# Optimization experiments

Hardware: AMD Instinct MI355X
Metric: run time of the kernel (lower is better)

## Reference

```python
import jax, jax.numpy as jnp
import numpy as np

B, S, D = 2, 1024, 768
H, DH = 12, 64
M = 64            # performer random features
DFF = 4 * D
EPS_LN = 1e-5
EPS_PHI = 1e-6


def setup_inputs() -> dict:
    key = jax.random.key(0)
    ks = jax.random.split(key, 12)
    std = 0.02
    return {
        "x": jax.random.normal(ks[0], (B, S, D), jnp.float32),
        "ln1_g": jnp.ones((D,), jnp.float32),
        "ln1_b": jnp.zeros((D,), jnp.float32),
        "w_attn": jax.random.normal(ks[1], (D, 3 * D), jnp.float32) * std,
        "b_attn": jnp.zeros((3 * D,), jnp.float32),
        "w_feat": jax.random.normal(ks[2], (M, DH), jnp.float32),  # FAVOR+ projection
        "w_proj": jax.random.normal(ks[3], (D, D), jnp.float32) * std,
        "b_proj": jnp.zeros((D,), jnp.float32),
        "ln2_g": jnp.ones((D,), jnp.float32),
        "ln2_b": jnp.zeros((D,), jnp.float32),
        "w_fc": jax.random.normal(ks[4], (D, DFF), jnp.float32) * std,
        "b_fc": jnp.zeros((DFF,), jnp.float32),
        "w_out": jax.random.normal(ks[5], (DFF, D), jnp.float32) * std,
        "b_out": jnp.zeros((D,), jnp.float32),
    }


def _layernorm(x, g, b):
    mu = jnp.mean(x, axis=-1, keepdims=True)
    var = jnp.mean(jnp.square(x - mu), axis=-1, keepdims=True)
    return (x - mu) * jax.lax.rsqrt(var + EPS_LN) * g + b


def _phi(x, w_feat):
    # FAVOR+ positive softmax-kernel features. x: [B,H,S,DH] (already scaled by dh^-1/4)
    proj = jnp.einsum('bhsd,md->bhsm', x, w_feat)
    sq = 0.5 * jnp.sum(jnp.square(x), axis=-1, keepdims=True)
    return jnp.exp(proj - sq) / np.sqrt(M) + EPS_PHI


def _performer_attn(q, k, v, w_feat, w_proj, b_proj):
    # split heads: [B,S,D] -> [B,H,S,DH]
    def heads(t):
        return t.reshape(B, S, H, DH).transpose(0, 2, 1, 3)
    q, k, v = heads(q), heads(k), heads(v)
    scale = DH ** -0.25
    phi_q = _phi(q * scale, w_feat)  # [B,H,S,M]
    phi_k = _phi(k * scale, w_feat)
    # causal linear attention via prefix sums
    kv = jnp.cumsum(phi_k[..., :, None] * v[..., None, :], axis=2)  # [B,H,S,M,DH]
    num = jnp.einsum('bhsm,bhsmd->bhsd', phi_q, kv)
    den = jnp.einsum('bhsm,bhsm->bhs', phi_q, jnp.cumsum(phi_k, axis=2))
    out = num / den[..., None]
    out = out.transpose(0, 2, 1, 3).reshape(B, S, D)
    return out @ w_proj + b_proj


def reference(x, ln1_g, ln1_b, w_attn, b_attn, w_feat, w_proj, b_proj,
              ln2_g, ln2_b, w_fc, b_fc, w_out, b_out):
    a = _layernorm(x, ln1_g, ln1_b)
    qkv = a @ w_attn + b_attn                      # TFConv1D
    q, k, v = jnp.split(qkv, 3, axis=2)
    x = x + _performer_attn(q, k, v, w_feat, w_proj, b_proj)
    m = _layernorm(x, ln2_g, ln2_b)
    m = jax.nn.gelu(m @ w_fc + b_fc, approximate=True) @ w_out + b_out
    return x + m
```

## Files before the change

kernel.cpp:

```cpp
#include <hip/hip_runtime.h>
#include <hip/hip_bf16.h>
#include <math.h>

#define BB 2
#define SS 1024
#define DD 768
#define HH 12
#define DHH 64
#define MM 64
#define DFF 3072
#define BS (BB*SS)
#define EPS_LN 1e-5f
#define EPS_PHI 1e-6f
#define CC 64
#define NC (SS/CC)
#define NQ 3840
#define PQOFF 2304
#define PKOFF 3072
#define VOFF  1536

typedef __hip_bfloat16 bf16;
using v8s = __attribute__((ext_vector_type(8))) short;
using v4f = __attribute__((ext_vector_type(4))) float;
struct b4 { bf16 v[4]; };

typedef const __attribute__((address_space(1))) void ga_void;
typedef __attribute__((address_space(3))) void ls_void;
__device__ __forceinline__ void gload16(const void* g, void* l) {
    __builtin_amdgcn_global_load_lds((ga_void*)g, (ls_void*)l, 16, 0, 0);
}

__global__ __launch_bounds__(256) void prep_kernel(const float* __restrict__ w_attn,
                                                   const float* __restrict__ w_proj,
                                                   const float* __restrict__ w_fc,
                                                   const float* __restrict__ w_out,
                                                   const float* __restrict__ b_attn,
                                                   const float* __restrict__ wfeat,
                                                   bf16* __restrict__ wext_t,
                                                   bf16* __restrict__ wproj_t,
                                                   bf16* __restrict__ wfc_t,
                                                   bf16* __restrict__ wout_t,
                                                   float* __restrict__ bias_ext) {
    __shared__ float smem[2 * 64 * 65];
    int bid = blockIdx.x;
    int t = threadIdx.x;
    if (bid < 1728) {
        const float* in; bf16* outp; int K, N, xt, yt;
        if (bid < 432)       { in = w_attn; outp = wext_t;  K = 768;  N = 2304; xt = bid % 36; yt = bid / 36; }
        else if (bid < 576)  { int b = bid - 432;  in = w_proj; outp = wproj_t; K = 768;  N = 768;  xt = b % 12; yt = b / 12; }
        else if (bid < 1152) { int b = bid - 576;  in = w_fc;   outp = wfc_t;   K = 768;  N = 3072; xt = b % 48; yt = b / 48; }
        else                 { int b = bid - 1152; in = w_out;  outp = wout_t;  K = 3072; N = 768;  xt = b % 12; yt = b / 12; }
        float (*sm)[65] = (float(*)[65])smem;
        int n0 = xt * 64, k0 = yt * 64;
        int rr = t >> 4, cc = (t & 15) * 4;
        #pragma unroll
        for (int it = 0; it < 4; it++) {
            int kr = it * 16 + rr;
            float4 v = *(const float4*)&in[(size_t)(k0 + kr) * N + n0 + cc];
            sm[kr][cc + 0] = v.x; sm[kr][cc + 1] = v.y;
            sm[kr][cc + 2] = v.z; sm[kr][cc + 3] = v.w;
        }
        __syncthreads();
        #pragma unroll
        for (int it = 0; it < 4; it++) {
            int nr = it * 16 + rr;
            b4 o;
            #pragma unroll
            for (int j = 0; j < 4; j++) o.v[j] = __float2bfloat16(sm[cc + j][nr]);
            *(b4*)&outp[(size_t)(n0 + nr) * K + k0 + cc] = o;
        }
    } else if (bid < 2016) {
        int b2 = bid - 1728;
        int jb = b2 % 12, h = (b2 / 12) % 12, isK = b2 / 144;
        float (*wfT)[65] = (float(*)[65])smem;
        float (*Wt)[65]  = (float(*)[65])(smem + 64 * 65);
        int j0 = jb * 64;
        int base = isK * DD + h * DHH;
        const float scale = 0.35355339059327373f;
        #pragma unroll
        for (int it = 0; it < 16; it++) {
            int idx = it * 256 + t;
            int m = idx >> 6, d = idx & 63;
            wfT[d][m] = scale * wfeat[m * DHH + d];
            Wt[idx >> 6][idx & 63] = w_attn[(size_t)(j0 + (idx >> 6)) * (3 * DD) + base + (idx & 63)];
        }
        __syncthreads();
        int jl = t & 63, mg = (t >> 6) * 16;
        for (int m = mg; m < mg + 16; m++) {
            float acc = 0.f;
            #pragma unroll 8
            for (int d = 0; d < 64; d++) acc += wfT[d][m] * Wt[jl][d];
            wext_t[(size_t)(PQOFF + isK * DD + h * DHH + m) * DD + j0 + jl] = __float2bfloat16(acc);
        }
        if (jb == 0 && t < 64) {
            float accb = 0.f;
            #pragma unroll 8
            for (int d = 0; d < 64; d++) accb += wfT[d][t] * b_attn[base + d];
            bias_ext[PQOFF + isK * DD + h * DHH + t] = accb;
        }
    } else {
        for (int i = t; i < 3 * DD; i += 256) bias_ext[i] = b_attn[i];
    }
}

__global__ __launch_bounds__(256) void ln_kernel(const float* __restrict__ x,
                                                 const float* __restrict__ g,
                                                 const float* __restrict__ bta,
                                                 bf16* __restrict__ out) {
    int row = blockIdx.x;
    int t = threadIdx.x;
    const float* xr = x + (size_t)row * DD;
    float v0 = xr[t], v1 = xr[t + 256], v2 = xr[t + 512];
    float s = v0 + v1 + v2;
    float s2 = v0 * v0 + v1 * v1 + v2 * v2;
    #pragma unroll
    for (int off = 32; off > 0; off >>= 1) {
        s  += __shfl_xor(s,  off, 64);
        s2 += __shfl_xor(s2, off, 64);
    }
    __shared__ float ls[4], ls2[4];
    if ((t & 63) == 0) { ls[t >> 6] = s; ls2[t >> 6] = s2; }
    __syncthreads();
    s  = ls[0] + ls[1] + ls[2] + ls[3];
    s2 = ls2[0] + ls2[1] + ls2[2] + ls2[3];
    float mu  = s * (1.0f / DD);
    float var = s2 * (1.0f / DD) - mu * mu;
    float r = rsqrtf(var + EPS_LN);
    bf16* orow = out + (size_t)row * DD;
    orow[t]       = __float2bfloat16((v0 - mu) * r * g[t]       + bta[t]);
    orow[t + 256] = __float2bfloat16((v1 - mu) * r * g[t + 256] + bta[t + 256]);
    orow[t + 512] = __float2bfloat16((v2 - mu) * r * g[t + 512] + bta[t + 512]);
}

__device__ inline void swizzle44(int bid, int nx4, int& bx, int& by) {
    int g = bid >> 4, r = bid & 15;
    bx = (g % nx4) * 4 + (r & 3);
    by = (g / nx4) * 4 + (r >> 2);
}

__device__ inline float gelu_tanh(float x) {
    float x3 = x * x * x;
    float u = 0.7978845608028654f * (x + 0.044715f * x3);
    return 0.5f * x * (1.0f + tanhf(u));
}

template <int ACT, int HAS_RES, int OUT_BF16>
__global__ __launch_bounds__(256) void gemm_k128(const bf16* __restrict__ A,
                                                 const bf16* __restrict__ BT,
                                                 const float* __restrict__ bias,
                                                 const float* __restrict__ res,
                                                 void* __restrict__ Cout,
                                                 int N, int K, int nx4) {
    __shared__ bf16 Asl[64][128];
    __shared__ bf16 Bsl[64][128];
    int bx, by;
    swizzle44(blockIdx.x, nx4, bx, by);
    int tid = threadIdx.x;
    int m0 = by * 64, n0 = bx * 64;
    int wave = tid >> 6, lane = tid & 63;
    int qm = lane & 15, quad = lane >> 4;
    int srow = lane >> 4;
    int chnk = lane & 15;
    int sce = (chnk ^ srow) * 8;
    int sco = (chnk ^ (srow + 4)) * 8;
    const bf16* ag = A  + (size_t)(m0 + wave * 16 + srow) * K;
    const bf16* bg = BT + (size_t)(n0 + wave * 16 + srow) * K;
    int xr = (qm & 7) << 3;

    v4f acc[4] = {{0.f,0.f,0.f,0.f},{0.f,0.f,0.f,0.f},{0.f,0.f,0.f,0.f},{0.f,0.f,0.f,0.f}};

    for (int k0 = 0; k0 < K; k0 += 128) {
        __syncthreads();
        #pragma unroll
        for (int i = 0; i < 4; i++) {
            int sc = (i & 1) ? sco : sce;
            gload16(ag + (size_t)(4 * i) * K + k0 + sc, &Asl[wave * 16 + 4 * i][0]);
            gload16(bg + (size_t)(4 * i) * K + k0 + sc, &Bsl[wave * 16 + 4 * i][0]);
        }
        __syncthreads();
        #pragma unroll
        for (int kc = 0; kc < 4; kc++) {
            v8s a = *(const v8s*)&Asl[wave * 16 + qm][(kc * 32 + quad * 8) ^ xr];
            #pragma unroll
            for (int n = 0; n < 4; n++) {
                v8s b = *(const v8s*)&Bsl[n * 16 + qm][(kc * 32 + quad * 8) ^ xr];
                acc[n] = __builtin_amdgcn_mfma_f32_16x16x32_bf16(a, b, acc[n], 0, 0, 0);
            }
        }
    }

    int col_l = lane & 15;
    #pragma unroll
    for (int t = 0; t < 4; t++) {
        int col = n0 + t * 16 + col_l;
        float bcol = bias[col];
        #pragma unroll
        for (int r = 0; r < 4; r++) {
            int row = m0 + wave * 16 + quad * 4 + r;
            float v = acc[t][r] + bcol;
            if (ACT == 1) v = gelu_tanh(v);
            if (HAS_RES) v += res[(size_t)row * N + col];
            if (OUT_BF16) ((bf16*)Cout)[(size_t)row * N + col] = __float2bfloat16(v);
            else          ((float*)Cout)[(size_t)row * N + col] = v;
        }
    }
}

template <int ACT, int HAS_RES, int OUT_BF16>
__global__ __launch_bounds__(256) void gemm_m32_k128(const bf16* __restrict__ A,
                                                     const bf16* __restrict__ BT,
                                                     const float* __restrict__ bias,
                                                     const float* __restrict__ res,
                                                     void* __restrict__ Cout,
                                                     int N, int K, int nx4) {
    __shared__ bf16 Asl[32][128];
    __shared__ bf16 Bsl[64][128];
    int bx, by;
    swizzle44(blockIdx.x, nx4, bx, by);
    int tid = threadIdx.x;
    int m0 = by * 32, n0 = bx * 64;
    int wave = tid >> 6, lane = tid & 63;
    int qm = lane & 15, quad = lane >> 4;
    int rowh = (wave & 1) * 16;
    int colh = (wave >> 1) * 32;
    int srow = lane >> 4;
    int chnk = lane & 15;
    int sce = (chnk ^ srow) * 8;
    int sco = (chnk ^ (srow + 4)) * 8;
    const bf16* ag = A  + (size_t)(m0 + wave * 8  + srow) * K;
    const bf16* bg = BT + (size_t)(n0 + wave * 16 + srow) * K;
    int xr = (qm & 7) << 3;

    v4f acc[2] = {{0.f,0.f,0.f,0.f},{0.f,0.f,0.f,0.f}};

    for (int k0 = 0; k0 < K; k0 += 128) {
        __syncthreads();
        #pragma unroll
        for (int i = 0; i < 2; i++) {
            int sc = (i & 1) ? sco : sce;
            gload16(ag + (size_t)(4 * i) * K + k0 + sc, &Asl[wave * 8 + 4 * i][0]);
        }
        #pragma unroll
        for (int i = 0; i < 4; i++) {
            int sc = (i & 1) ? sco : sce;
            gload16(bg + (size_t)(4 * i) * K + k0 + sc, &Bsl[wave * 16 + 4 * i][0]);
        }
        __syncthreads();
        #pragma unroll
        for (int kc = 0; kc < 4; kc++) {
            v8s a  = *(const v8s*)&Asl[rowh + qm][(kc * 32 + quad * 8) ^ xr];
            v8s b0 = *(const v8s*)&Bsl[colh + qm][(kc * 32 + quad * 8) ^ xr];
            v8s b1 = *(const v8s*)&Bsl[colh + 16 + qm][(kc * 32 + quad * 8) ^ xr];
            acc[0] = __builtin_amdgcn_mfma_f32_16x16x32_bf16(a, b0, acc[0], 0, 0, 0);
            acc[1] = __builtin_amdgcn_mfma_f32_16x16x32_bf16(a, b1, acc[1], 0, 0, 0);
        }
    }

    #pragma unroll
    for (int ct = 0; ct < 2; ct++) {
        int col = n0 + colh + ct * 16 + qm;
        float bcol = bias[col];
        #pragma unroll
        for (int r = 0; r < 4; r++) {
            int row = m0 + rowh + quad * 4 + r;
            float v = acc[ct][r] + bcol;
            if (ACT == 1) v = gelu_tanh(v);
            if (HAS_RES) v += res[(size_t)row * N + col];
            if (OUT_BF16) ((bf16*)Cout)[(size_t)row * N + col] = __float2bfloat16(v);
            else          ((float*)Cout)[(size_t)row * N + col] = v;
        }
    }
}

__device__ __forceinline__ float rowsq16(b4 raw) {
    float sq = 0.f;
    #pragma unroll
    for (int j = 0; j < 4; j++) { float f = __bfloat162float(raw.v[j]); sq += f * f; }
    sq += __shfl_xor(sq, 1, 64); sq += __shfl_xor(sq, 2, 64);
    sq += __shfl_xor(sq, 4, 64); sq += __shfl_xor(sq, 8, 64);
    return sq * (1.0f / 16.0f);
}

__global__ __launch_bounds__(256) void scan_sums_mfma(const bf16* __restrict__ qkvp,
                                                      float* __restrict__ StateT,
                                                      float* __restrict__ Sk) {
    int c = blockIdx.x, h = blockIdx.y, b = blockIdx.z;
    int bh = b * HH + h;
    int t = threadIdx.x;
    __shared__ bf16 vt[64][72];
    __shared__ bf16 kt[64][72];
    int sr = t >> 4, cq = (t & 15) * 4;
    #pragma unroll
    for (int i = 0; i < 4; i++) {
        int s = sr + 16 * i;
        size_t rowg = ((size_t)b * SS + c * CC + s) * NQ + h * DHH;
        b4 vv = *(const b4*)&qkvp[rowg + VOFF  + cq];
        b4 kr = *(const b4*)&qkvp[rowg + DD    + cq];
        b4 kp = *(const b4*)&qkvp[rowg + PKOFF + cq];
        float sq = rowsq16(kr);
        #pragma unroll
        for (int j = 0; j < 4; j++) {
            vt[cq + j][s] = vv.v[j];
            kt[cq + j][s] = __float2bfloat16(
                __expf(__bfloat162float(kp.v[j]) - sq) * 0.125f + EPS_PHI);
        }
    }
    __syncthreads();
    int wave = t >> 6, lane = t & 63, qm = lane & 15, quad = lane >> 4;
    v4f acc[4] = {{0.f,0.f,0.f,0.f},{0.f,0.f,0.f,0.f},{0.f,0.f,0.f,0.f},{0.f,0.f,0.f,0.f}};
    #pragma unroll
    for (int k0 = 0; k0 < 64; k0 += 32) {
        v8s a = *(const v8s*)&vt[wave * 16 + qm][k0 + quad * 8];
        #pragma unroll
        for (int n = 0; n < 4; n++) {
            v8s bb = *(const v8s*)&kt[n * 16 + qm][k0 + quad * 8];
            acc[n] = __builtin_amdgcn_mfma_f32_16x16x32_bf16(a, bb, acc[n], 0, 0, 0);
        }
    }
    float* dst = StateT + ((size_t)bh * NC + c) * 4096;
    int col_l = lane & 15;
    #pragma unroll
    for (int n = 0; n < 4; n++)
        #pragma unroll
        for (int r = 0; r < 4; r++) {
            int d = wave * 16 + quad * 4 + r;
            dst[d * 64 + n * 16 + col_l] = acc[n][r];
        }
    if (t < 64) {
        float sum = 0.f;
        #pragma unroll 8
        for (int i = 0; i < 64; i++) sum += __bfloat162float(kt[t][i]);
        Sk[((size_t)bh * NC + c) * 64 + t] = sum;
    }
}

__global__ __launch_bounds__(256) void scan_prefix_kernel(float* __restrict__ Skv,
                                                          float* __restrict__ Sk) {
    int bh = blockIdx.y;
    int t = blockIdx.x * 256 + threadIdx.x;
    size_t base = (size_t)bh * NC * 4096 + t;
    float acc = 0.f;
    for (int c = 0; c < NC; c++) {
        float v = Skv[base + (size_t)c * 4096];
        Skv[base + (size_t)c * 4096] = acc;
        acc += v;
    }
    if (blockIdx.x == 0 && threadIdx.x < 64) {
        size_t b2 = (size_t)bh * NC * 64 + threadIdx.x;
        float a2 = 0.f;
        for (int c = 0; c < NC; c++) {
            float v = Sk[b2 + (size_t)c * 64];
            Sk[b2 + (size_t)c * 64] = a2;
            a2 += v;
        }
    }
}

__global__ __launch_bounds__(256) void scan_chunk_mfma(const bf16* __restrict__ qkvp,
                                                       const float* __restrict__ StateT,
                                                       const float* __restrict__ SkPre,
                                                       bf16* __restrict__ attn) {
    int c = blockIdx.x, h = blockIdx.y, b = blockIdx.z;
    int bh = b * HH + h;
    int t = threadIdx.x;
    __shared__ bf16 qs[64][72];
    __shared__ bf16 ks[64][72];
    __shared__ bf16 vt[80][72];
    __shared__ bf16 stl[80][72];
    __shared__ bf16 P[64][72];
    int sr = t >> 4, cq = (t & 15) * 4;
    const float* stg = StateT + ((size_t)bh * NC + c) * 4096;
    #pragma unroll
    for (int i = 0; i < 4; i++) {
        int s = sr + 16 * i;
        size_t rowg = ((size_t)b * SS + c * CC + s) * NQ + h * DHH;
        b4 qr = *(const b4*)&qkvp[rowg + 0     + cq];
        b4 qp = *(const b4*)&qkvp[rowg + PQOFF + cq];
        b4 kr = *(const b4*)&qkvp[rowg + DD    + cq];
        b4 kp = *(const b4*)&qkvp[rowg + PKOFF + cq];
        b4 vv = *(const b4*)&qkvp[rowg + VOFF  + cq];
        float4 sv = *(const float4*)&stg[s * 64 + cq];
        float sqq = rowsq16(qr);
        float sqk = rowsq16(kr);
        #pragma unroll
        for (int j = 0; j < 4; j++) {
            qs[s][cq + j] = __float2bfloat16(
                __expf(__bfloat162float(qp.v[j]) - sqq) * 0.125f + EPS_PHI);
            ks[s][cq + j] = __float2bfloat16(
                __expf(__bfloat162float(kp.v[j]) - sqk) * 0.125f + EPS_PHI);
            vt[cq + j][s] = vv.v[j];
        }
        stl[s][cq + 0] = __float2bfloat16(sv.x);
        stl[s][cq + 1] = __float2bfloat16(sv.y);
        stl[s][cq + 2] = __float2bfloat16(sv.z);
        stl[s][cq + 3] = __float2bfloat16(sv.w);
    }
    {
        int rr = 64 + (t >> 4);
        bf16 one = __float2bfloat16(rr == 64 ? 1.f : 0.f);
        vt[rr][cq + 0] = one; vt[rr][cq + 1] = one;
        vt[rr][cq + 2] = one; vt[rr][cq + 3] = one;
        if (rr == 64) {
            const float* skp = SkPre + ((size_t)bh * NC + c) * 64;
            float4 s4 = *(const float4*)&skp[cq];
            stl[64][cq + 0] = __float2bfloat16(s4.x);
            stl[64][cq + 1] = __float2bfloat16(s4.y);
            stl[64][cq + 2] = __float2bfloat16(s4.z);
            stl[64][cq + 3] = __float2bfloat16(s4.w);
        } else {
            bf16 z = __float2bfloat16(0.f);
            stl[rr][cq + 0] = z; stl[rr][cq + 1] = z;
            stl[rr][cq + 2] = z; stl[rr][cq + 3] = z;
        }
    }
    __syncthreads();
    int wave = t >> 6, lane = t & 63, qm = lane & 15, quad = lane >> 4;
    int col_l = lane & 15;
    int row0 = wave * 16;

    v4f a1[4] = {{0.f,0.f,0.f,0.f},{0.f,0.f,0.f,0.f},{0.f,0.f,0.f,0.f},{0.f,0.f,0.f,0.f}};
    #pragma unroll
    for (int k0 = 0; k0 < 64; k0 += 32) {
        v8s a = *(const v8s*)&qs[row0 + qm][k0 + quad * 8];
        #pragma unroll
        for (int n = 0; n < 4; n++) {
            v8s bb = *(const v8s*)&ks[n * 16 + qm][k0 + quad * 8];
            a1[n] = __builtin_amdgcn_mfma_f32_16x16x32_bf16(a, bb, a1[n], 0, 0, 0);
        }
    }
    #pragma unroll
    for (int n = 0; n < 4; n++)
        #pragma unroll
        for (int r = 0; r < 4; r++) {
            int row = row0 + quad * 4 + r;
            int col = n * 16 + col_l;
            float v = (col <= row) ? a1[n][r] : 0.f;
            P[row][col] = __float2bfloat16(v);
        }
    v4f acc[5] = {{0.f,0.f,0.f,0.f},{0.f,0.f,0.f,0.f},{0.f,0.f,0.f,0.f},
                  {0.f,0.f,0.f,0.f},{0.f,0.f,0.f,0.f}};
    #pragma unroll
    for (int k0 = 0; k0 < 64; k0 += 32) {
        v8s aq = *(const v8s*)&qs[row0 + qm][k0 + quad * 8];
        v8s ap = *(const v8s*)&P [row0 + qm][k0 + quad * 8];
        #pragma unroll
        for (int n = 0; n < 5; n++) {
            v8s b1 = *(const v8s*)&stl[n * 16 + qm][k0 + quad * 8];
            v8s b2 = *(const v8s*)&vt [n * 16 + qm][k0 + quad * 8];
            acc[n] = __builtin_amdgcn_mfma_f32_16x16x32_bf16(aq, b1, acc[n], 0, 0, 0);
            acc[n] = __builtin_amdgcn_mfma_f32_16x16x32_bf16(ap, b2, acc[n], 0, 0, 0);
        }
    }
    float den[4];
    #pragma unroll
    for (int r = 0; r < 4; r++)
        den[r] = __shfl(acc[4][r], (lane >> 4) << 4, 64);
    #pragma unroll
    for (int n = 0; n < 4; n++)
        #pragma unroll
        for (int r = 0; r < 4; r++) {
            int srow = row0 + quad * 4 + r;
            int d = n * 16 + col_l;
            attn[((size_t)b * SS + c * CC + srow) * DD + h * DHH + d] =
                __float2bfloat16(acc[n][r] / den[r]);
        }
}

extern "C" void kernel_launch(void* const* d_in, const int* in_sizes, int n_in,
                              void* d_out, int out_size, void* d_ws, size_t ws_size,
                              hipStream_t stream) {
    const float* x      = (const float*)d_in[0];
    const float* ln1_g  = (const float*)d_in[1];
    const float* ln1_b  = (const float*)d_in[2];
    const float* w_attn = (const float*)d_in[3];
    const float* b_attn = (const float*)d_in[4];
    const float* w_feat = (const float*)d_in[5];
    const float* w_proj = (const float*)d_in[6];
    const float* b_proj = (const float*)d_in[7];
    const float* ln2_g  = (const float*)d_in[8];
    const float* ln2_b  = (const float*)d_in[9];
    const float* w_fc   = (const float*)d_in[10];
    const float* b_fc   = (const float*)d_in[11];
    const float* w_out  = (const float*)d_in[12];
    const float* b_out  = (const float*)d_in[13];
    float* out = (float*)d_out;

    float* ws = (float*)d_ws;
    size_t off = 0;
    float* buf_x1   = ws + off; off += (size_t)BS * DD;
    float* buf_sk   = ws + off; off += (size_t)BB * HH * NC * MM;
    float* bias_ext = ws + off; off += NQ;
    bf16* wb = (bf16*)(ws + off);
    size_t boff = 0;
    bf16* buf_qkvp    = wb + boff; boff += (size_t)BS * NQ;
    bf16* buf_a_bf    = wb + boff; boff += (size_t)BS * DD;
    bf16* buf_attn_bf = wb + boff; boff += (size_t)BS * DD;
    bf16* wext_t      = wb + boff; boff += (size_t)NQ * DD;
    bf16* wproj_t     = wb + boff; boff += (size_t)DD * DD;
    bf16* wfc_t       = wb + boff; boff += (size_t)DFF * DD;
    bf16* wout_t      = wb + boff; boff += (size_t)DD * DFF;
    float* buf_skv   = buf_x1;
    bf16*  buf_fc_bf = buf_qkvp;

    prep_kernel<<<2017, 256, 0, stream>>>(w_attn, w_proj, w_fc, w_out, b_attn, w_feat,
                                          wext_t, wproj_t, wfc_t, wout_t, bias_ext);
    ln_kernel<<<BS, 256, 0, stream>>>(x, ln1_g, ln1_b, buf_a_bf);
    gemm_k128<0, 0, 1><<<1920, 256, 0, stream>>>(
        buf_a_bf, wext_t, bias_ext, nullptr, buf_qkvp, NQ, DD, 15);
    scan_sums_mfma<<<dim3(NC, HH, BB), 256, 0, stream>>>(buf_qkvp, buf_skv, buf_sk);
    scan_prefix_kernel<<<dim3(4096 / 256, BB * HH), 256, 0, stream>>>(buf_skv, buf_sk);
    scan_chunk_mfma<<<dim3(NC, HH, BB), 256, 0, stream>>>(
        buf_qkvp, buf_skv, buf_sk, buf_attn_bf);
    gemm_m32_k128<0, 1, 0><<<768, 256, 0, stream>>>(
        buf_attn_bf, wproj_t, b_proj, x, buf_x1, DD, DD, 3);
    ln_kernel<<<BS, 256, 0, stream>>>(buf_x1, ln2_g, ln2_b, buf_a_bf);
    gemm_k128<1, 0, 1><<<1536, 256, 0, stream>>>(
        buf_a_bf, wfc_t, b_fc, nullptr, buf_fc_bf, DFF, DD, 12);
    gemm_m32_k128<0, 1, 0><<<768, 256, 0, stream>>>(
        buf_fc_bf, wout_t, b_out, buf_x1, out, DD, DFF, 3);
}
```

Measured before the change: 227.9 us.

## Fuse LN1 into prep, emit q/k squared norms from QKV GEMM epilogue

New measurement: 227.9 us. No clear change (-0.0%).

```diff
diff --git a/kernel.cpp b/kernel.cpp
--- a/kernel.cpp
+++ b/kernel.cpp
@@ -30,12 +30,16 @@
     __builtin_amdgcn_global_load_lds((ga_void*)g, (ls_void*)l, 16, 0, 0);
 }
 
-__global__ __launch_bounds__(256) void prep_kernel(const float* __restrict__ w_attn,
+__global__ __launch_bounds__(256) void prep_kernel(const float* __restrict__ x,
+                                                   const float* __restrict__ ln1_g,
+                                                   const float* __restrict__ ln1_b,
+                                                   const float* __restrict__ w_attn,
                                                    const float* __restrict__ w_proj,
                                                    const float* __restrict__ w_fc,
                                                    const float* __restrict__ w_out,
                                                    const float* __restrict__ b_attn,
                                                    const float* __restrict__ wfeat,
+                                                   bf16* __restrict__ a_bf,
                                                    bf16* __restrict__ wext_t,
                                                    bf16* __restrict__ wproj_t,
                                                    bf16* __restrict__ wfc_t,
@@ -44,12 +48,36 @@
     __shared__ float smem[2 * 64 * 65];
     int bid = blockIdx.x;
     int t = threadIdx.x;
-    if (bid < 1728) {
+    if (bid < 2048) {
+        int row = bid;
+        const float* xr = x + (size_t)row * DD;
+        float v0 = xr[t], v1 = xr[t + 256], v2 = xr[t + 512];
+        float s = v0 + v1 + v2;
+        float s2 = v0 * v0 + v1 * v1 + v2 * v2;
+        #pragma unroll
+        for (int off = 32; off > 0; off >>= 1) {
+            s  += __shfl_xor(s,  off, 64);
+            s2 += __shfl_xor(s2, off, 64);
+        }
+        float* ls = smem; float* ls2 = smem + 4;
+        if ((t & 63) == 0) { ls[t >> 6] = s; ls2[t >> 6] = s2; }
+        __syncthreads();
+        s  = ls[0] + ls[1] + ls[2] + ls[3];
+        s2 = ls2[0] + ls2[1] + ls2[2] + ls2[3];
+        float mu  = s * (1.0f / DD);
+        float var = s2 * (1.0f / DD) - mu * mu;
+        float r = rsqrtf(var + EPS_LN);
+        bf16* orow = a_bf + (size_t)row * DD;
+        orow[t]       = __float2bfloat16((v0 - mu) * r * ln1_g[t]       + ln1_b[t]);
+        orow[t + 256] = __float2bfloat16((v1 - mu) * r * ln1_g[t + 256] + ln1_b[t + 256]);
+        orow[t + 512] = __float2bfloat16((v2 - mu) * r * ln1_g[t + 512] + ln1_b[t + 512]);
+    } else if (bid < 3776) {
+        int b = bid - 2048;
         const float* in; bf16* outp; int K, N, xt, yt;
-        if (bid < 432)       { in = w_attn; outp = wext_t;  K = 768;  N = 2304; xt = bid % 36; yt = bid / 36; }
-        else if (bid < 576)  { int b = bid - 432;  in = w_proj; outp = wproj_t; K = 768;  N = 768;  xt = b % 12; yt = b / 12; }
-        else if (bid < 1152) { int b = bid - 576;  in = w_fc;   outp = wfc_t;   K = 768;  N = 3072; xt = b % 48; yt = b / 48; }
-        else                 { int b = bid - 1152; in = w_out;  outp = wout_t;  K = 3072; N = 768;  xt = b % 12; yt = b / 12; }
+        if (b < 432)       { in = w_attn; outp = wext_t;  K = 768;  N = 2304; xt = b % 36; yt = b / 36; }
+        else if (b < 576)  { int b1 = b - 432;  in = w_proj; outp = wproj_t; K = 768;  N = 768;  xt = b1 % 12; yt = b1 / 12; }
+        else if (b < 1152) { int b1 = b - 576;  in = w_fc;   outp = wfc_t;   K = 768;  N = 3072; xt = b1 % 48; yt = b1 / 48; }
+        else               { int b1 = b - 1152; in = w_out;  outp = wout_t;  K = 3072; N = 768;  xt = b1 % 12; yt = b1 / 12; }
         float (*sm)[65] = (float(*)[65])smem;
         int n0 = xt * 64, k0 = yt * 64;
         int rr = t >> 4, cc = (t & 15) * 4;
@@ -69,8 +97,8 @@
             for (int j = 0; j < 4; j++) o.v[j] = __float2bfloat16(sm[cc + j][nr]);
             *(b4*)&outp[(size_t)(n0 + nr) * K + k0 + cc] = o;
         }
-    } else if (bid < 2016) {
-        int b2 = bid - 1728;
+    } else if (bid < 4064) {
+        int b2 = bid - 3776;
         int jb = b2 % 12, h = (b2 / 12) % 12, isK = b2 / 144;
         float (*wfT)[65] = (float(*)[65])smem;
         float (*Wt)[65]  = (float(*)[65])(smem + 64 * 65);
@@ -144,13 +172,14 @@
     return 0.5f * x * (1.0f + tanhf(u));
 }
 
-template <int ACT, int HAS_RES, int OUT_BF16>
+template <int ACT, int HAS_RES, int OUT_BF16, int SQMODE>
 __global__ __launch_bounds__(256) void gemm_k128(const bf16* __restrict__ A,
                                                  const bf16* __restrict__ BT,
                                                  const float* __restrict__ bias,
                                                  const float* __restrict__ res,
                                                  void* __restrict__ Cout,
-                                                 int N, int K, int nx4) {
+                                                 int N, int K, int nx4,
+                                                 float* __restrict__ sqbuf) {
     __shared__ bf16 Asl[64][128];
     __shared__ bf16 Bsl[64][128];
     int bx, by;
@@ -190,14 +219,33 @@
     }
 
     int col_l = lane & 15;
-    #pragma unroll
-    for (int t = 0; t < 4; t++) {
-        int col = n0 + t * 16 + col_l;
+    if (SQMODE && n0 < 1536) {
+        int hidx = n0 >> 6;
+        #pragma unroll
+        for (int r = 0; r < 4; r++) {
+            float hsq = 0.f;
+            #pragma unroll
+            for (int t2 = 0; t2 < 4; t2++) {
+                float v = acc[t2][r] + bias[n0 + t2 * 16 + col_l];
+                hsq += v * v;
+            }
+            hsq += __shfl_xor(hsq, 1, 64); hsq += __shfl_xor(hsq, 2, 64);
+            hsq += __shfl_xor(hsq, 4, 64); hsq += __shfl_xor(hsq, 8, 64);
+            if (col_l == 0) {
+                int row = m0 + wave * 16 + quad * 4 + r;
+                sqbuf[row * 24 + hidx] = hsq * (1.0f / 16.0f);
+            }
+        }
+        return;
+    }
+    #pragma unroll
+    for (int t2 = 0; t2 < 4; t2++) {
+        int col = n0 + t2 * 16 + col_l;
         float bcol = bias[col];
         #pragma unroll
         for (int r = 0; r < 4; r++) {
             int row = m0 + wave * 16 + quad * 4 + r;
-            float v = acc[t][r] + bcol;
+            float v = acc[t2][r] + bcol;
             if (ACT == 1) v = gelu_tanh(v);
             if (HAS_RES) v += res[(size_t)row * N + col];
             if (OUT_BF16) ((bf16*)Cout)[(size_t)row * N + col] = __float2bfloat16(v);
@@ -272,16 +320,8 @@
     }
 }
 
-__device__ __forceinline__ float rowsq16(b4 raw) {
-    float sq = 0.f;
-    #pragma unroll
-    for (int j = 0; j < 4; j++) { float f = __bfloat162float(raw.v[j]); sq += f * f; }
-    sq += __shfl_xor(sq, 1, 64); sq += __shfl_xor(sq, 2, 64);
-    sq += __shfl_xor(sq, 4, 64); sq += __shfl_xor(sq, 8, 64);
-    return sq * (1.0f / 16.0f);
-}
-
 __global__ __launch_bounds__(256) void scan_sums_mfma(const bf16* __restrict__ qkvp,
+                                                      const float* __restrict__ sqbuf,
                                                       float* __restrict__ StateT,
                                                       float* __restrict__ Sk) {
     int c = blockIdx.x, h = blockIdx.y, b = blockIdx.z;
@@ -293,11 +333,11 @@
     #pragma unroll
     for (int i = 0; i < 4; i++) {
         int s = sr + 16 * i;
-        size_t rowg = ((size_t)b * SS + c * CC + s) * NQ + h * DHH;
+        size_t grow = (size_t)b * SS + c * CC + s;
+        size_t rowg = grow * NQ + h * DHH;
         b4 vv = *(const b4*)&qkvp[rowg + VOFF  + cq];
-        b4 kr = *(const b4*)&qkvp[rowg + DD    + cq];
         b4 kp = *(const b4*)&qkvp[rowg + PKOFF + cq];
-        float sq = rowsq16(kr);
+        float sq = sqbuf[grow * 24 + 12 + h];
         #pragma unroll
         for (int j = 0; j < 4; j++) {
             vt[cq + j][s] = vv.v[j];
@@ -326,11 +366,14 @@
             int d = wave * 16 + quad * 4 + r;
             dst[d * 64 + n * 16 + col_l] = acc[n][r];
         }
-    if (t < 64) {
+    {
+        int m = t >> 2, j = t & 3;
         float sum = 0.f;
-        #pragma unroll 8
-        for (int i = 0; i < 64; i++) sum += __bfloat162float(kt[t][i]);
-        Sk[((size_t)bh * NC + c) * 64 + t] = sum;
+        #pragma unroll
+        for (int i2 = 0; i2 < 16; i2++) sum += __bfloat162float(kt[m][j * 16 + i2]);
+        sum += __shfl_xor(sum, 1, 64);
+        sum += __shfl_xor(sum, 2, 64);
+        if (j == 0) Sk[((size_t)bh * NC + c) * 64 + m] = sum;
     }
 }
 
@@ -357,6 +400,7 @@
 }
 
 __global__ __launch_bounds__(256) void scan_chunk_mfma(const bf16* __restrict__ qkvp,
+                                                       const float* __restrict__ sqbuf,
                                                        const float* __restrict__ StateT,
                                                        const float* __restrict__ SkPre,
                                                        bf16* __restrict__ attn) {
@@ -365,23 +409,22 @@
     int t = threadIdx.x;
     __shared__ bf16 qs[64][72];
     __shared__ bf16 ks[64][72];
-    __shared__ bf16 vt[80][72];
-    __shared__ bf16 stl[80][72];
+    __shared__ bf16 vt[64][72];
+    __shared__ bf16 stl[64][72];
     __shared__ bf16 P[64][72];
     int sr = t >> 4, cq = (t & 15) * 4;
     const float* stg = StateT + ((size_t)bh * NC + c) * 4096;
     #pragma unroll
     for (int i = 0; i < 4; i++) {
         int s = sr + 16 * i;
-        size_t rowg = ((size_t)b * SS + c * CC + s) * NQ + h * DHH;
-        b4 qr = *(const b4*)&qkvp[rowg + 0     + cq];
+        size_t grow = (size_t)b * SS + c * CC + s;
+        size_t rowg = grow * NQ + h * DHH;
         b4 qp = *(const b4*)&qkvp[rowg + PQOFF + cq];
-        b4 kr = *(const b4*)&qkvp[rowg + DD    + cq];
         b4 kp = *(const b4*)&qkvp[rowg + PKOFF + cq];
         b4 vv = *(const b4*)&qkvp[rowg + VOFF  + cq];
         float4 sv = *(const float4*)&stg[s * 64 + cq];
-        float sqq = rowsq16(qr);
-        float sqk = rowsq16(kr);
+        float sqq = sqbuf[grow * 24 + h];
+        float sqk = sqbuf[grow * 24 + 12 + h];
         #pragma unroll
         for (int j = 0; j < 4; j++) {
             qs[s][cq + j] = __float2bfloat16(
@@ -395,24 +438,6 @@
         stl[s][cq + 2] = __float2bfloat16(sv.z);
         stl[s][cq + 3] = __float2bfloat16(sv.w);
     }
-    {
-        int rr = 64 + (t >> 4);
-        bf16 one = __float2bfloat16(rr == 64 ? 1.f : 0.f);
-        vt[rr][cq + 0] = one; vt[rr][cq + 1] = one;
-        vt[rr][cq + 2] = one; vt[rr][cq + 3] = one;
-        if (rr == 64) {
-            const float* skp = SkPre + ((size_t)bh * NC + c) * 64;
-            float4 s4 = *(const float4*)&skp[cq];
-            stl[64][cq + 0] = __float2bfloat16(s4.x);
-            stl[64][cq + 1] = __float2bfloat16(s4.y);
-            stl[64][cq + 2] = __float2bfloat16(s4.z);
-            stl[64][cq + 3] = __float2bfloat16(s4.w);
-        } else {
-            bf16 z = __float2bfloat16(0.f);
-            stl[rr][cq + 0] = z; stl[rr][cq + 1] = z;
-            stl[rr][cq + 2] = z; stl[rr][cq + 3] = z;
-        }
-    }
     __syncthreads();
     int wave = t >> 6, lane = t & 63, qm = lane & 15, quad = lane >> 4;
     int col_l = lane & 15;
@@ -428,6 +453,7 @@
             a1[n] = __builtin_amdgcn_mfma_f32_16x16x32_bf16(a, bb, a1[n], 0, 0, 0);
         }
     }
+    float denl[4] = {0.f, 0.f, 0.f, 0.f};
     #pragma unroll
     for (int n = 0; n < 4; n++)
         #pragma unroll
@@ -436,25 +462,41 @@
             int col = n * 16 + col_l;
             float v = (col <= row) ? a1[n][r] : 0.f;
             P[row][col] = __float2bfloat16(v);
-        }
-    v4f acc[5] = {{0.f,0.f,0.f,0.f},{0.f,0.f,0.f,0.f},{0.f,0.f,0.f,0.f},
-                  {0.f,0.f,0.f,0.f},{0.f,0.f,0.f,0.f}};
+            denl[r] += v;
+        }
+    {
+        const float* skp = SkPre + ((size_t)bh * NC + c) * 64;
+        float4 sk4 = *(const float4*)&skp[qm * 4];
+        #pragma unroll
+        for (int r = 0; r < 4; r++) {
+            int row = row0 + quad * 4 + r;
+            b4 qv = *(const b4*)&qs[row][qm * 4];
+            denl[r] += __bfloat162float(qv.v[0]) * sk4.x
+                     + __bfloat162float(qv.v[1]) * sk4.y
+                     + __bfloat162float(qv.v[2]) * sk4.z
+                     + __bfloat162float(qv.v[3]) * sk4.w;
+        }
+    }
+    #pragma unroll
+    for (int r = 0; r < 4; r++) {
+        denl[r] += __shfl_xor(denl[r], 1, 64);
+        denl[r] += __shfl_xor(denl[r], 2, 64);
+        denl[r] += __shfl_xor(denl[r], 4, 64);
+        denl[r] += __shfl_xor(denl[r], 8, 64);
+    }
+    v4f acc[4] = {{0.f,0.f,0.f,0.f},{0.f,0.f,0.f,0.f},{0.f,0.f,0.f,0.f},{0.f,0.f,0.f,0.f}};
     #pragma unroll
     for (int k0 = 0; k0 < 64; k0 += 32) {
         v8s aq = *(const v8s*)&qs[row0 + qm][k0 + quad * 8];
         v8s ap = *(const v8s*)&P [row0 + qm][k0 + quad * 8];
         #pragma unroll
-        for (int n = 0; n < 5; n++) {
+        for (int n = 0; n < 4; n++) {
             v8s b1 = *(const v8s*)&stl[n * 16 + qm][k0 + quad * 8];
             v8s b2 = *(const v8s*)&vt [n * 16 + qm][k0 + quad * 8];
             acc[n] = __builtin_amdgcn_mfma_f32_16x16x32_bf16(aq, b1, acc[n], 0, 0, 0);
             acc[n] = __builtin_amdgcn_mfma_f32_16x16x32_bf16(ap, b2, acc[n], 0, 0, 0);
         }
     }
-    float den[4];
-    #pragma unroll
-    for (int r = 0; r < 4; r++)
-        den[r] = __shfl(acc[4][r], (lane >> 4) << 4, 64);
     #pragma unroll
     for (int n = 0; n < 4; n++)
         #pragma unroll
@@ -462,7 +504,7 @@
             int srow = row0 + quad * 4 + r;
             int d = n * 16 + col_l;
             attn[((size_t)b * SS + c * CC + srow) * DD + h * DHH + d] =
-                __float2bfloat16(acc[n][r] / den[r]);
+                __float2bfloat16(acc[n][r] / denl[r]);
         }
 }
 
@@ -490,6 +532,7 @@
     float* buf_x1   = ws + off; off += (size_t)BS * DD;
     float* buf_sk   = ws + off; off += (size_t)BB * HH * NC * MM;
     float* bias_ext = ws + off; off += NQ;
+    float* buf_sq   = ws + off; off += (size_t)BS * 24;
     bf16* wb = (bf16*)(ws + off);
     size_t boff = 0;
     bf16* buf_qkvp    = wb + boff; boff += (size_t)BS * NQ;
@@ -502,20 +545,20 @@
     float* buf_skv   = buf_x1;
     bf16*  buf_fc_bf = buf_qkvp;
 
-    prep_kernel<<<2017, 256, 0, stream>>>(w_attn, w_proj, w_fc, w_out, b_attn, w_feat,
-                                          wext_t, wproj_t, wfc_t, wout_t, bias_ext);
-    ln_kernel<<<BS, 256, 0, stream>>>(x, ln1_g, ln1_b, buf_a_bf);
-    gemm_k128<0, 0, 1><<<1920, 256, 0, stream>>>(
-        buf_a_bf, wext_t, bias_ext, nullptr, buf_qkvp, NQ, DD, 15);
-    scan_sums_mfma<<<dim3(NC, HH, BB), 256, 0, stream>>>(buf_qkvp, buf_skv, buf_sk);
+    prep_kernel<<<4065, 256, 0, stream>>>(x, ln1_g, ln1_b,
+                                          w_attn, w_proj, w_fc, w_out, b_attn, w_feat,
+                                          buf_a_bf, wext_t, wproj_t, wfc_t, wout_t, bias_ext);
+    gemm_k128<0, 0, 1, 1><<<1920, 256, 0, stream>>>(
+        buf_a_bf, wext_t, bias_ext, nullptr, buf_qkvp, NQ, DD, 15, buf_sq);
+    scan_sums_mfma<<<dim3(NC, HH, BB), 256, 0, stream>>>(buf_qkvp, buf_sq, buf_skv, buf_sk);
     scan_prefix_kernel<<<dim3(4096 / 256, BB * HH), 256, 0, stream>>>(buf_skv, buf_sk);
     scan_chunk_mfma<<<dim3(NC, HH, BB), 256, 0, stream>>>(
-        buf_qkvp, buf_skv, buf_sk, buf_attn_bf);
+        buf_qkvp, buf_sq, buf_skv, buf_sk, buf_attn_bf);
     gemm_m32_k128<0, 1, 0><<<768, 256, 0, stream>>>(
         buf_attn_bf, wproj_t, b_proj, x, buf_x1, DD, DD, 3);
     ln_kernel<<<BS, 256, 0, stream>>>(buf_x1, ln2_g, ln2_b, buf_a_bf);
-    gemm_k128<1, 0, 1><<<1536, 256, 0, stream>>>(
-        buf_a_bf, wfc_t, b_fc, nullptr, buf_fc_bf, DFF, DD, 12);
+    gemm_k128<1, 0, 1, 0><<<1536, 256, 0, stream>>>(
+        buf_a_bf, wfc_t, b_fc, nullptr, buf_fc_bf, DFF, DD, 12, nullptr);
     gemm_m32_k128<0, 1, 0><<<768, 256, 0, stream>>>(
         buf_fc_bf, wout_t, b_out, buf_x1, out, DD, DFF, 3);
 }
```
